# Optimization experiments

Hardware: AMD Instinct MI355X
Metric: run time of the kernel (lower is better)

Reference implementation:

```python
import jax, jax.numpy as jnp
import numpy as np

FS = 24000.0
C_SOUND = 343.0
MAX_TAU = 6
IGNORE = -100
PAIRS = np.array([(0, 1), (0, 2), (0, 3), (1, 2), (1, 3), (2, 3)])  # m1<m2 loop order
PERMS_NP = np.array([(0, 1, 2), (0, 2, 1), (1, 0, 2), (1, 2, 0), (2, 0, 1), (2, 1, 0)])  # itertools order


def _mic_locs():
    # [rad, azi_deg, ele_deg] per mic, centered at origin (matches center_mic_coords)
    coords = np.array([[0.042, 45, 35], [0.042, -45, -35], [0.042, 135, -35], [0.042, -135, 35]], dtype=np.float64)
    rad = coords[:, 0]
    azi = coords[:, 1] * 2 * np.pi / 360
    ele = coords[:, 2] * 2 * np.pi / 360
    locs = np.stack([rad * np.cos(azi) * np.cos(ele), rad * np.sin(azi) * np.cos(ele), rad * np.sin(ele)], axis=1)
    return jnp.asarray(locs, dtype=jnp.float32)

MIC_LOCS = _mic_locs()  # [4,3]


def _get_tdoa_targets(target):
    """Vectorized get_tdoa_target. target: [B,T,E,5,C].
    Assumes <=1 active class per (b,t,track) so the random class shuffle is a no-op.
    Returns (tdoas, tdoas2) as int32 [B,T,E,6]."""
    B, T, E, F, C = target.shape
    active = target[:, :, :, 0, :]                                  # [B,T,E,C] 0/1 flags
    is_active = jnp.any(active > 0, axis=-1)                        # [B,T,E]
    doa = jnp.einsum('btec,btedc->bted', active, target[:, :, :, 1:4, :])  # [B,T,E,3]
    dist = jnp.einsum('btec,btec->bte', active, target[:, :, :, 4, :])     # [B,T,E]
    src = doa * dist[..., None]                                     # [B,T,E,3]
    d = jnp.linalg.norm(src[..., None, :] - MIC_LOCS, axis=-1)      # [B,T,E,4] dist to each mic
    tdoa = d[..., PAIRS[:, 0]] - d[..., PAIRS[:, 1]]                # [B,T,E,6]
    tdoa = jnp.round(tdoa * FS / C_SOUND) + MAX_TAU                 # [B,T,E,6]
    # compact active tracks to the front (stable keeps track order, matching tr_cnt)
    order = jnp.argsort(jnp.logical_not(is_active), axis=-1)        # [B,T,E]
    gathered = jnp.take_along_axis(tdoa, order[..., None], axis=2)  # [B,T,E,6]
    n = jnp.sum(is_active, axis=-1)                                 # [B,T] number of events
    k = jnp.arange(E)[None, None, :]                                # slot index
    idx1 = jnp.clip(jnp.minimum(k, n[:, :, None] - 1), 0, E - 1)    # pad with LAST event
    idx2 = jnp.where(k < n[:, :, None], k, 0)                       # pad with FIRST event
    tdoas = jnp.take_along_axis(gathered, idx1[..., None], axis=2)
    tdoas2 = jnp.take_along_axis(gathered, idx2[..., None], axis=2)
    empty = (n == 0)[:, :, None, None]
    tdoas = jnp.where(empty, float(IGNORE), tdoas)
    tdoas2 = jnp.where(empty, float(IGNORE), tdoas2)
    return tdoas.astype(jnp.int32), tdoas2.astype(jnp.int32)


def _forward(pred, t_a, t_b):
    B, T, C, Tr, ntd = pred.shape
    N = B * T * ntd
    p = pred.transpose(0, 1, 4, 2, 3).reshape(N, C, Tr)             # [N,C,Tr]
    ta = t_a.transpose(0, 1, 3, 2).reshape(N, Tr)                   # [N,Tr]
    tb = t_b.transpose(0, 1, 3, 2).reshape(N, Tr)
    logp = jax.nn.log_softmax(p, axis=1)                            # [N,C,Tr]
    perms = jnp.asarray(PERMS_NP)                                   # [6,Tr]
    ar = jnp.arange(Tr)

    def pit(t):
        tc = jnp.clip(t, 0, C - 1)
        # L[n,i,j] = CE(pred track j, target track i); ignore_index -> 0
        L = -jnp.take_along_axis(logp, jnp.broadcast_to(tc[:, :, None], (N, Tr, Tr)), axis=1)
        L = jnp.where((t == IGNORE)[:, :, None], 0.0, L)
        pl = L[:, ar[None, :], perms].mean(axis=-1)                 # [N,6] per-perm mean loss
        pidx = jnp.argmin(pl, axis=1)                               # first min (matches torch loop)
        return jnp.take_along_axis(pl, pidx[:, None], axis=1)[:, 0], perms[pidx]

    loss1, perm1 = pit(ta)
    loss2, perm2 = pit(tb)
    use2 = loss2 < loss1                                            # torch.min keeps first on ties
    loss = jnp.where(use2, loss2, loss1)
    t_sel = jnp.where(use2[:, None], tb, ta)
    perm_sel = jnp.where(use2[:, None], perm2, perm1)

    pred_cls = jnp.argmax(p, axis=1)                                # [N,Tr]
    t_perm = jnp.take_along_axis(t_sel, perm_sel, axis=1)           # target reordered by opt perm
    valid = t_perm != IGNORE
    npred = jnp.sum(valid)
    correct = jnp.sum((pred_cls == t_perm) & valid)
    acc = jnp.where(npred > 0, correct.astype(jnp.float32) / jnp.maximum(npred, 1).astype(jnp.float32), 0.0)

    mask = loss > 0.0
    nval = jnp.sum(mask)
    lmean = jnp.where(nval > 0, jnp.sum(jnp.where(mask, loss, 0.0)) / jnp.maximum(nval, 1).astype(loss.dtype), 0.0)
    return lmean, acc


def setup_inputs() -> dict:
    key = jax.random.key(0)
    B, T, E, NCLS, NTD, CPRED = 128, 600, 3, 13, 6, 13
    k1, k2, k3, k4, k5 = jax.random.split(key, 5)
    pred = jax.random.normal(k1, (B, T, CPRED, E, NTD), dtype=jnp.float32)
    act_cls = jax.random.randint(k2, (B, T, E), 0, NCLS)
    act_flag = (jax.random.uniform(k3, (B, T, E)) < 0.5).astype(jnp.float32)
    onehot = jax.nn.one_hot(act_cls, NCLS, dtype=jnp.float32) * act_flag[..., None]  # <=1 active class/track
    doa = jax.random.normal(k4, (B, T, E, 3), dtype=jnp.float32)
    doa = doa / jnp.linalg.norm(doa, axis=-1, keepdims=True)
    dist = jax.random.uniform(k5, (B, T, E), minval=1.0, maxval=3.0, dtype=jnp.float32)
    target = jnp.concatenate([
        onehot[:, :, :, None, :],
        jnp.broadcast_to(doa[..., None], (B, T, E, 3, NCLS)),
        jnp.broadcast_to(dist[..., None, None], (B, T, E, 1, NCLS)),
    ], axis=3).astype(jnp.float32)                                  # [B,T,E,5,NCLS]
    return {"pred": pred, "target": target}


def reference(pred, target):
    t_a, t_b = _get_tdoa_targets(target)
    return _forward(pred, t_a, t_b)
```

## Files before the change

kernel.cpp:

```cpp
#include <hip/hip_runtime.h>
#include <cstdint>
#include <cstddef>

#define BT_TOTAL 76800
#define NITEMS   (BT_TOTAL * 6)
#define NTHR     256
#define NBLK     (NITEMS / NTHR)
#define NCLS     13
#define IGN      (-100)

struct Partial { float ls; int lc; int cor; int val; };

extern "C" __global__ __launch_bounds__(NTHR, 5)
void tdoa_flat(const float* __restrict__ pred, const float* __restrict__ target,
               Partial* __restrict__ part) {
    const int tid  = threadIdx.x;
    const int gid  = blockIdx.x * NTHR + tid;
    const int cell = gid / 6;
    const int p    = gid - cell * 6;

    const float* tg = target + (size_t)cell * 195;
    const float* pp = pred   + (size_t)cell * 234 + p;

    const float MX[4] = { 0.02432757455f,  0.02432757455f, -0.02432757455f, -0.02432757455f };
    const float MY[4] = { 0.02432757455f, -0.02432757455f,  0.02432757455f, -0.02432757455f };
    const float MZ[4] = { 0.02409021033f, -0.02409021033f, -0.02409021033f,  0.02409021033f };
    const int PI_[6] = {0,0,0,1,1,2};
    const int PJ_[6] = {1,2,3,2,3,3};
    const int mi = PI_[p], mj = PJ_[p];
    const float mxi = MX[mi], myi = MY[mi], mzi = MZ[mi];
    const float mxj = MX[mj], myj = MY[mj], mzj = MZ[mj];

    int  td[3];
    bool ab[3];
    int  nact = 0;
#pragma unroll
    for (int e = 0; e < 3; e++) {
        float av = 0.f; int ci = 0; bool ia = false;
#pragma unroll
        for (int c = 0; c < NCLS; c++) {
            const float a = tg[e * 65 + c];
            const bool  g = (a > 0.0f);
            av = g ? a : av;
            ci = g ? c : ci;
            ia = ia || g;
        }
        const float d0 = av * tg[e * 65 + 13 + ci];
        const float d1 = av * tg[e * 65 + 26 + ci];
        const float d2 = av * tg[e * 65 + 39 + ci];
        const float ds = av * tg[e * 65 + 52 + ci];
        const float sx = d0 * ds, sy = d1 * ds, sz = d2 * ds;
        const float exi = sx - mxi, eyi = sy - myi, ezi = sz - mzi;
        const float exj = sx - mxj, eyj = sy - myj, ezj = sz - mzj;
        const float dmi = sqrtf(exi * exi + eyi * eyi + ezi * ezi);
        const float dmj = sqrtf(exj * exj + eyj * eyj + ezj * ezj);
        td[e] = (int)rintf((dmi - dmj) * (24000.0f / 343.0f)) + 6;
        ab[e] = ia;
        nact += ia ? 1 : 0;
    }

    const int g0 = ab[0] ? td[0] : (ab[1] ? td[1] : td[2]);
    const int g1 = (ab[0] && ab[1]) ? td[1] : td[2];
    const int g2 = td[2];
    int ta[3], tb[3];
    ta[0] = g0;
    ta[1] = (nact >= 2) ? g1 : g0;
    ta[2] = (nact == 3) ? g2 : ((nact == 2) ? g1 : g0);
    tb[0] = g0;
    tb[1] = (nact >= 2) ? g1 : g0;
    tb[2] = (nact == 3) ? g2 : g0;
    if (nact == 0) { ta[0] = ta[1] = ta[2] = IGN; tb[0] = tb[1] = tb[2] = IGN; }

    float x[NCLS][3];
#pragma unroll
    for (int c = 0; c < NCLS; c++)
#pragma unroll
        for (int j = 0; j < 3; j++)
            x[c][j] = pp[c * 18 + j * 6];

    int   am[3];
    float lse[3];
#pragma unroll
    for (int j = 0; j < 3; j++) {
        float m = x[0][j]; int a = 0;
#pragma unroll
        for (int c = 1; c < NCLS; c++) { if (x[c][j] > m) { m = x[c][j]; a = c; } }
        float s = 0.f;
#pragma unroll
        for (int c = 0; c < NCLS; c++) s += expf(x[c][j] - m);
        am[j] = a; lse[j] = m + logf(s);
    }

    float La[3][3], Lb[3][3];
#pragma unroll
    for (int i = 0; i < 3; i++) {
        const int  ca  = (ta[i] < 0) ? 0 : ta[i];
        const int  cbb = (tb[i] < 0) ? 0 : tb[i];
        const bool ia2 = (ta[i] == IGN);
        const bool ib2 = (tb[i] == IGN);
#pragma unroll
        for (int j = 0; j < 3; j++) {
            La[i][j] = ia2 ? 0.f : (lse[j] - pp[ca  * 18 + j * 6]);
            Lb[i][j] = ib2 ? 0.f : (lse[j] - pp[cbb * 18 + j * 6]);
        }
    }

    const int P0[6] = {0,0,1,1,2,2};
    const int P1[6] = {1,2,0,2,0,1};
    const int P2[6] = {2,1,2,0,1,0};
    float l1 = 0.f, l2 = 0.f; int i1 = 0, i2 = 0;
#pragma unroll
    for (int q = 0; q < 6; q++) {
        const float va = (La[0][P0[q]] + La[1][P1[q]] + La[2][P2[q]]) * (1.0f / 3.0f);
        const float vb = (Lb[0][P0[q]] + Lb[1][P1[q]] + Lb[2][P2[q]]) * (1.0f / 3.0f);
        if (q == 0) { l1 = va; l2 = vb; }
        else {
            if (va < l1) { l1 = va; i1 = q; }
            if (vb < l2) { l2 = vb; i2 = q; }
        }
    }

    const bool use2 = (l2 < l1);
    const float loss = use2 ? l2 : l1;
    const int  qsel = use2 ? i2 : i1;
    const int PK[6] = {36, 24, 33, 9, 18, 6};
    int pk = PK[0];
#pragma unroll
    for (int k = 1; k < 6; k++) pk = (qsel == k) ? PK[k] : pk;
    const int s0 = use2 ? tb[0] : ta[0];
    const int s1 = use2 ? tb[1] : ta[1];
    const int s2 = use2 ? tb[2] : ta[2];

    float lsum = 0.f;
    int   lcnt = 0, cor = 0, nval = 0;
#pragma unroll
    for (int i = 0; i < 3; i++) {
        const int pi = (pk >> (2 * i)) & 3;
        const int tp = (pi == 0) ? s0 : ((pi == 1) ? s1 : s2);
        const bool v = (tp != IGN);
        nval += v ? 1 : 0;
        cor  += (v && (am[i] == tp)) ? 1 : 0;
    }
    if (loss > 0.f) { lsum += loss; lcnt++; }

#pragma unroll
    for (int off = 32; off > 0; off >>= 1) {
        lsum += __shfl_down(lsum, off, 64);
        lcnt += __shfl_down(lcnt, off, 64);
        cor  += __shfl_down(cor,  off, 64);
        nval += __shfl_down(nval, off, 64);
    }
    __shared__ float rf[4];
    __shared__ int   r1[4], r2[4], r3[4];
    const int wid = tid >> 6;
    if ((tid & 63) == 0) { rf[wid] = lsum; r1[wid] = lcnt; r2[wid] = cor; r3[wid] = nval; }
    __syncthreads();
    if (tid == 0) {
        Partial pt;
        pt.ls  = rf[0] + rf[1] + rf[2] + rf[3];
        pt.lc  = r1[0] + r1[1] + r1[2] + r1[3];
        pt.cor = r2[0] + r2[1] + r2[2] + r2[3];
        pt.val = r3[0] + r3[1] + r3[2] + r3[3];
        part[blockIdx.x] = pt;
    }
}

extern "C" __global__ __launch_bounds__(256)
void tdoa_final(const Partial* __restrict__ part, float* __restrict__ out) {
    const int tid = threadIdx.x;
    double ls = 0.0; int lc = 0, cor = 0, val = 0;
    for (int i = tid; i < NBLK; i += 256) {
        const Partial p = part[i];
        ls += (double)p.ls; lc += p.lc; cor += p.cor; val += p.val;
    }
#pragma unroll
    for (int off = 32; off > 0; off >>= 1) {
        ls  += __shfl_down(ls,  off, 64);
        lc  += __shfl_down(lc,  off, 64);
        cor += __shfl_down(cor, off, 64);
        val += __shfl_down(val, off, 64);
    }
    __shared__ double sd[4];
    __shared__ int    s1[4], s2[4], s3[4];
    const int wid = tid >> 6;
    if ((tid & 63) == 0) { sd[wid] = ls; s1[wid] = lc; s2[wid] = cor; s3[wid] = val; }
    __syncthreads();
    if (tid == 0) {
        const double L = sd[0] + sd[1] + sd[2] + sd[3];
        const int c1 = s1[0] + s1[1] + s1[2] + s1[3];
        const int c2 = s2[0] + s2[1] + s2[2] + s2[3];
        const int c3 = s3[0] + s3[1] + s3[2] + s3[3];
        out[0] = (c1 > 0) ? (float)(L / (double)c1) : 0.0f;
        out[1] = (c3 > 0) ? ((float)c2 / (float)c3) : 0.0f;
    }
}

extern "C" void kernel_launch(void* const* d_in, const int* in_sizes, int n_in,
                              void* d_out, int out_size, void* d_ws, size_t ws_size,
                              hipStream_t stream) {
    const float* pred   = (const float*)d_in[0];
    const float* target = (const float*)d_in[1];
    Partial* part = (Partial*)d_ws;
    float* out = (float*)d_out;
    hipLaunchKernelGGL(tdoa_flat,  dim3(NBLK), dim3(NTHR), 0, stream, pred, target, part);
    hipLaunchKernelGGL(tdoa_final, dim3(1),    dim3(256), 0, stream, part, out);
}
```

Measured before the change: 180.6 us.

## Stage pred tiles into LDS with async global_load_lds, 32 cells per block

Each block now handles 32 cells with 192 threads and copies the block's contiguous pred slab into shared memory as 16-byte chunks using the async global-to-LDS load builtin. Per-thread strided gathers (stride 18 floats) then read from LDS instead of global memory, and the target decode overlaps the in-flight copy before a barrier. The intent is fully coalesced wide reads of pred in place of scattered 4-byte loads. The cost is about 30KB of LDS per block, which limits occupancy, plus an extra barrier.

```diff
diff --git a/kernel.cpp b/kernel.cpp
--- a/kernel.cpp
+++ b/kernel.cpp
@@ -3,24 +3,46 @@
 #include <cstddef>
 
 #define BT_TOTAL 76800
-#define NITEMS   (BT_TOTAL * 6)
-#define NTHR     256
-#define NBLK     (NITEMS / NTHR)
-#define NCLS     13
-#define IGN      (-100)
+#define NCLS 13
+#define IGN  (-100)
+
+#define CPB   32
+#define NTHR  192
+#define NBLK  (BT_TOTAL / CPB)
+#define NF4P  (CPB * 234 / 4)
+#define KP    10
+#define PADP  (KP * NTHR)
 
 struct Partial { float ls; int lc; int cor; int val; };
 
-extern "C" __global__ __launch_bounds__(NTHR, 5)
-void tdoa_flat(const float* __restrict__ pred, const float* __restrict__ target,
-               Partial* __restrict__ part) {
-    const int tid  = threadIdx.x;
-    const int gid  = blockIdx.x * NTHR + tid;
-    const int cell = gid / 6;
-    const int p    = gid - cell * 6;
-
-    const float* tg = target + (size_t)cell * 195;
-    const float* pp = pred   + (size_t)cell * 234 + p;
+__device__ __forceinline__ void stage16(const float4* g, float4* l) {
+    __builtin_amdgcn_global_load_lds((const __attribute__((address_space(1))) void*)g,
+                                     (__attribute__((address_space(3))) void*)l,
+                                     16, 0, 0);
+}
+
+extern "C" __global__ __launch_bounds__(NTHR)
+void tdoa_fused(const float* __restrict__ pred, const float* __restrict__ target,
+                Partial* __restrict__ part) {
+    const int tid = threadIdx.x;
+    const int cb  = blockIdx.x * CPB;
+
+    __shared__ float4 sP4[PADP];
+    const float* sP = (const float*)sP4;
+
+    {
+        const float4* gp = (const float4*)(pred + (size_t)cb * 234);
+#pragma unroll
+        for (int r = 0; r < KP; r++) {
+            const int i  = r * NTHR + tid;
+            const int ic = (i < NF4P) ? i : (NF4P - 1);
+            stage16(gp + ic, &sP4[i]);
+        }
+    }
+
+    const int cell = tid / 6;
+    const int p    = tid - cell * 6;
+    const float* tg = target + (size_t)(cb + cell) * 195;
 
     const float MX[4] = { 0.02432757455f,  0.02432757455f, -0.02432757455f, -0.02432757455f };
     const float MY[4] = { 0.02432757455f, -0.02432757455f,  0.02432757455f, -0.02432757455f };
@@ -71,6 +93,10 @@
     tb[2] = (nact == 3) ? g2 : g0;
     if (nact == 0) { ta[0] = ta[1] = ta[2] = IGN; tb[0] = tb[1] = tb[2] = IGN; }
 
+    __syncthreads();
+
+    const float* pp = sP + cell * 234 + p;
+
     float x[NCLS][3];
 #pragma unroll
     for (int c = 0; c < NCLS; c++)
@@ -150,17 +176,17 @@
         cor  += __shfl_down(cor,  off, 64);
         nval += __shfl_down(nval, off, 64);
     }
-    __shared__ float rf[4];
-    __shared__ int   r1[4], r2[4], r3[4];
+    __shared__ float rf[3];
+    __shared__ int   r1[3], r2[3], r3[3];
     const int wid = tid >> 6;
     if ((tid & 63) == 0) { rf[wid] = lsum; r1[wid] = lcnt; r2[wid] = cor; r3[wid] = nval; }
     __syncthreads();
     if (tid == 0) {
         Partial pt;
-        pt.ls  = rf[0] + rf[1] + rf[2] + rf[3];
-        pt.lc  = r1[0] + r1[1] + r1[2] + r1[3];
-        pt.cor = r2[0] + r2[1] + r2[2] + r2[3];
-        pt.val = r3[0] + r3[1] + r3[2] + r3[3];
+        pt.ls  = rf[0] + rf[1] + rf[2];
+        pt.lc  = r1[0] + r1[1] + r1[2];
+        pt.cor = r2[0] + r2[1] + r2[2];
+        pt.val = r3[0] + r3[1] + r3[2];
         part[blockIdx.x] = pt;
     }
 }
@@ -202,6 +228,6 @@
     const float* target = (const float*)d_in[1];
     Partial* part = (Partial*)d_ws;
     float* out = (float*)d_out;
-    hipLaunchKernelGGL(tdoa_flat,  dim3(NBLK), dim3(NTHR), 0, stream, pred, target, part);
+    hipLaunchKernelGGL(tdoa_fused, dim3(NBLK), dim3(NTHR), 0, stream, pred, target, part);
     hipLaunchKernelGGL(tdoa_final, dim3(1),    dim3(256), 0, stream, part, out);
 }
```

Measured after the change: 156.0 us. 1.16x faster.
